# Kernel tuning notes

Hardware: AMD Instinct MI355X
Metric: run time of the kernel (lower is better)

Reference implementation:

```python
import jax, jax.numpy as jnp
import numpy as np
from jax.scipy.special import gammaln

D = 512       # feature_dim
C = 64        # n classes (n-way)
SHOTS = 5     # matches hardcoded self.fix_Nj = 5
Q = 2048      # query samples
FIX_NJ = 5.0


def setup_inputs() -> dict:
    key = jax.random.key(0)
    k1, k2 = jax.random.split(key, 2)
    X_support = jax.random.normal(k1, (C * SHOTS, D), dtype=jnp.float32)
    # labels 0..C-1, SHOTS contiguous samples per class (required: code indexes mu[j] by label)
    y = (jnp.arange(C * SHOTS, dtype=jnp.int32) // SHOTS)
    X_query = jax.random.normal(k2, (Q, D), dtype=jnp.float32)
    # learned parameters, initialized exactly as in the torch module
    m = jnp.zeros((1, D), dtype=jnp.float32)
    kappa = jnp.float32(0.1)
    nu = jnp.float32(D)
    triu_S_diag = jnp.ones((D,), dtype=jnp.float32)
    triu_S_lower = jnp.eye(D, dtype=jnp.float32)
    return {"X_support": X_support, "y": y, "X_query": X_query,
            "m": m, "kappa": kappa, "nu": nu,
            "triu_S_diag": triu_S_diag, "triu_S_lower": triu_S_lower}


def reference(X_support, y, X_query, m, kappa, nu, triu_S_diag, triu_S_lower):
    # ---- compute_shared_part ----
    # triu(ones,1).t() == strictly-lower-triangular mask
    mask = jnp.tril(jnp.ones((D, D), dtype=X_support.dtype), -1)
    L = jnp.diag(jnp.abs(triu_S_diag)) + triu_S_lower * mask
    kappa_n = jnp.abs(kappa) + 1e-6 + FIX_NJ
    m_with_weight = jnp.abs(kappa + 1e-6) / kappa_n * m          # [1,D]
    xmean_weight = FIX_NJ / kappa_n
    scatter = L @ L.T                                            # self_outer(L), square case
    sp = jnp.clip(nu, D - 1 + 1e-6) + FIX_NJ - D + 2             # sharedpart (scalar)
    bias_shared = gammaln(0.5 * (sp + D)) - gammaln(0.5 * sp) - 0.5 * D * jnp.log(sp)

    # ---- fit_image_label, batched over classes ----
    # y is arange//SHOTS so grouping X[y==j] == contiguous reshape
    Xc = X_support.reshape(C, SHOTS, D)                          # [C,S,D]
    x_mean = Xc.mean(axis=1)                                     # [C,D]
    mean_outer = jnp.einsum('csd,cse->cde', Xc, Xc) / SHOTS      # X_j^T X_j / N_j
    mu = m_with_weight + x_mean * xmean_weight                   # [C,D]
    dm = x_mean - m                                              # [C,D]; self_outer of [1,D] row -> outer product
    sigma = scatter[None] + mean_outer \
        + jnp.einsum('cd,ce->cde', dm, dm) * ((jnp.abs(kappa) + 1e-6) / kappa_n)
    sigma = sigma / ((kappa_n + 1) / (kappa_n * sp))             # [C,D,D]
    sigma_inv = jnp.linalg.inv(sigma)                            # batched inverse
    _, logdet = jnp.linalg.slogdet(sigma)                        # sigma is PD -> logdet
    biases = bias_shared - 0.5 * logdet                          # [C]

    # ---- predict, batched over queries and classes ----
    diff = X_query[:, None, :] - mu[None, :, :]                  # [Q,C,D]
    tmp = jnp.einsum('qcd,cde->qce', diff, sigma_inv)
    dist = jnp.sum(tmp * diff, axis=-1)                          # Mahalanobis [Q,C]
    return biases[None, :] - 0.5 * (sp + D) * jnp.log(1.0 + dist / sp)
```

## Files before the change

kernel.cpp:

```cpp
#include <hip/hip_runtime.h>
#include <math.h>

#define D 512
#define NC 64
#define NQ 2048

typedef unsigned short u16;
typedef __attribute__((ext_vector_type(8))) short bf8;
typedef __attribute__((ext_vector_type(4))) float f4;

#define OFF_S    0
#define OFF_ABH  32
#define OFF_ABL  (OFF_ABH + 655360)
#define OFF_LH   (OFF_ABL + 655360)
#define OFF_LL   (OFF_LH + 131072)
#define OFF_WH   (OFF_LL + 131072)
#define OFF_WL   (OFF_WH + 131072)
#define OFF_YYH  (OFF_WL + 131072)
#define OFF_YYL  (OFF_YYH + 655360)
#define OFF_AQ   (OFF_YYL + 655360)
#define OFF_GRAM (OFF_AQ + NQ)

#define GIX(i, j) ((i) * 7 - (i) * ((i) + 1) / 2 + (j))

__device__ inline float wred(float v) {
#pragma unroll
  for (int off = 32; off; off >>= 1) v += __shfl_down(v, off);
  return v;
}

__device__ inline void split2(float v, u16& h, u16& l) {
  unsigned u = __float_as_uint(v);
  h = (u16)(u >> 16);
  float hf = __uint_as_float(u & 0xFFFF0000u);
  float r = v - hf;
  unsigned ru = __float_as_uint(r);
  l = (u16)((ru + 0x7FFFu + ((ru >> 16) & 1u)) >> 16);
}

#define MPAD 68
template <int N>
__device__ inline void lds_mm(float (*M)[MPAD], int ar, int ac, int br, int bc,
                              int cr, int cc, bool neg) {
  const int T = N / 16;
  int tx = (threadIdx.x & 15) * T, ty = (threadIdx.x >> 4) * T;
  float acc[T][T];
#pragma unroll
  for (int i = 0; i < T; ++i)
#pragma unroll
    for (int j = 0; j < T; ++j) acc[i][j] = 0.f;
#pragma unroll 8
  for (int k = 0; k < N; ++k) {
    float a[T], b[T];
#pragma unroll
    for (int i = 0; i < T; ++i) a[i] = M[ar + ty + i][ac + k];
#pragma unroll
    for (int j = 0; j < T; ++j) b[j] = M[br + k][bc + tx + j];
#pragma unroll
    for (int i = 0; i < T; ++i)
#pragma unroll
      for (int j = 0; j < T; ++j) acc[i][j] += a[i] * b[j];
  }
#pragma unroll
  for (int i = 0; i < T; ++i)
#pragma unroll
    for (int j = 0; j < T; ++j)
      M[cr + ty + i][cc + tx + j] = neg ? -acc[i][j] : acc[i][j];
}

__global__ __launch_bounds__(256) void k_prep(const float* __restrict__ diag,
                                              const float* __restrict__ low,
                                              const float* __restrict__ Xs,
                                              const float* __restrict__ Xq,
                                              const float* __restrict__ m,
                                              const float* __restrict__ kp,
                                              const float* __restrict__ nup,
                                              u16* __restrict__ Lh, u16* __restrict__ Ll,
                                              u16* __restrict__ ABh, u16* __restrict__ ABl,
                                              u16* __restrict__ Wh, u16* __restrict__ Wl,
                                              float* __restrict__ S, float* __restrict__ aq,
                                              float* __restrict__ Gram) {
  __shared__ float M[64][MPAD];
  int bid = blockIdx.x, tid = threadIdx.x;
  if (bid < 1024) {
    int t = bid * 256 + tid;
    int i = t >> 9, j = t & 511;
    float v = (i == j) ? fabsf(diag[i]) : (i > j ? low[t] : 0.f);
    u16 hh, ll; split2(v, hh, ll);
    Lh[t] = hh; Ll[t] = ll;
    if (i < j) Wh[t] = 0;
  } else if (bid < 1088) {
    int c = bid - 1024;
    float kappa = kp[0];
    float kn = fabsf(kappa) + 1e-6f + 5.0f;
    float xw = 5.0f / kn;
    float mw = fabsf(kappa + 1e-6f) / kn;
    float sw = sqrtf((fabsf(kappa) + 1e-6f) / kn);
    const float is5 = 0.44721359549995793f;
    for (int d = tid; d < D; d += 256) {
      float x[5];
#pragma unroll
      for (int s = 0; s < 5; ++s) x[s] = Xs[(size_t)(c * 5 + s) * D + d];
      float xm = (x[0] + x[1] + x[2] + x[3] + x[4]) * 0.2f;
      float mv = m[d];
      float rowv[8];
#pragma unroll
      for (int s = 0; s < 5; ++s) rowv[s] = x[s] * is5;
      rowv[5] = sw * (xm - mv);
      rowv[6] = mw * mv + xw * xm;
      rowv[7] = 0.f;
#pragma unroll
      for (int s = 0; s < 8; ++s) {
        size_t gi = (size_t)(c * 8 + s) * D + d;
        u16 hh, ll; split2(rowv[s], hh, ll);
        ABh[gi] = hh; ABl[gi] = ll;
      }
    }
  } else if (bid == 1088) {
    for (int i = tid; i < NQ; i += 256) aq[i] = 0.f;
    for (int i = tid; i < NC * 28; i += 256) Gram[i] = 0.f;
    if (tid >= 64) return;
    float part = 0.f;
    for (int i = tid; i < D; i += 64) part += logf(fabsf(diag[i]));
    part = wred(part);
    if (tid != 0) return;
    float lda = 2.f * part;
    float kappa = kp[0], nu = nup[0];
    float kn = fabsf(kappa) + 1e-6f + 5.0f;
    float sp = fmaxf(nu, (float)(D - 1) + 1e-6f) + 5.0f - (float)D + 2.0f;
    float bias_shared = lgammaf(0.5f * (sp + (float)D)) - lgammaf(0.5f * sp)
                      - 0.5f * (float)D * logf(sp);
    float scale = kn * sp / (kn + 1.0f);
    S[3] = bias_shared;
    S[8] = 1.f / scale;
    S[9] = (float)D * logf(scale) + lda;
    S[10] = 0.5f * (sp + (float)D);
    S[11] = 1.f / sp;
  } else if (bid < 1601) {
    int idx = bid - 1089;
    size_t base = (size_t)512 * D + (size_t)idx * 2048;
    for (int i = tid; i < 2048; i += 256) {
      float v = Xq[(size_t)idx * 2048 + i];
      u16 hh, ll; split2(v, hh, ll);
      ABh[base + i] = hh; ABl[base + i] = ll;
    }
  } else {
    int p = (bid - 1601) * 64;
    for (int idx = tid; idx < 64 * 64; idx += 256) {
      int r = idx >> 6, c = idx & 63;
      float v;
      if (r == c)      v = fabsf(diag[p + r]);
      else if (r > c)  v = low[(size_t)(p + r) * D + p + c];
      else             v = 0.f;
      M[r][c] = v;
    }
    __syncthreads();
    {
      float x[16];
      int q = tid >> 4, col = tid & 15;
      if (tid < 64) {
        int b = q << 4;
#pragma unroll
        for (int i = 0; i < 16; ++i) {
          float acc = 0.f;
#pragma unroll
          for (int k = 0; k < i; ++k) acc += M[b + i][b + k] * x[k];
          x[i] = (((i == col) ? 1.f : 0.f) - acc) / M[b + i][b + i];
        }
      }
      __syncthreads();
      if (tid < 64) {
        int b = q << 4;
#pragma unroll
        for (int i = 0; i < 16; ++i) M[b + i][b + col] = x[i];
      }
      __syncthreads();
    }
    for (int pp = 0; pp < 2; ++pp) {
      int r0 = 32 * pp;
      lds_mm<16>(M, r0 + 16, r0, r0, r0, r0, r0 + 16, false);
    }
    __syncthreads();
    for (int pp = 0; pp < 2; ++pp) {
      int r0 = 32 * pp;
      lds_mm<16>(M, r0 + 16, r0 + 16, r0, r0 + 16, r0 + 16, r0, true);
    }
    __syncthreads();
    lds_mm<32>(M, 32, 0, 0, 0, 0, 32, false);
    __syncthreads();
    lds_mm<32>(M, 32, 32, 0, 32, 32, 0, true);
    __syncthreads();
    for (int idx = tid; idx < 64 * 64; idx += 256) {
      int r = idx >> 6, c = idx & 63;
      float v = (c > r) ? 0.f : M[r][c];
      u16 hh, ll; split2(v, hh, ll);
      size_t gi = (size_t)(p + r) * D + p + c;
      Wh[gi] = hh; Wl[gi] = ll;
    }
  }
}

__global__ __launch_bounds__(256) void k_solve(const u16* __restrict__ Lh,
                                               const u16* __restrict__ Ll,
                                               u16* __restrict__ Wh,
                                               u16* __restrict__ Wl) {
  __shared__ __align__(16) u16 XTh[32][520];
  __shared__ __align__(16) u16 XTl[32][520];
  __shared__ __align__(16) u16 STh[32][72];
  __shared__ __align__(16) u16 STl[32][72];
  int J = blockIdx.x;
  int i0 = J >> 1;
  int tid = threadIdx.x, w = tid >> 6, lane = tid & 63;
  int lr = lane & 15, kq = lane >> 4;
  for (int idx = tid; idx < 64 * 32; idx += 256) {
    int r = idx >> 5, c = idx & 31;
    size_t gi = (size_t)(64 * i0 + r) * D + 64 * i0 + (J & 1) * 32 + c;
    XTh[c][64 * i0 + r] = Wh[gi];
    XTl[c][64 * i0 + r] = Wl[gi];
  }
  __syncthreads();
  for (int i = i0 + 1; i < 8; ++i) {
    f4 acc[2];
    acc[0] = (f4){0.f, 0.f, 0.f, 0.f};
    acc[1] = (f4){0.f, 0.f, 0.f, 0.f};
    for (int k = i0; k < i; ++k) {
#pragma unroll
      for (int kk = 0; kk < 2; ++kk) {
        size_t ga = (size_t)(64 * i + w * 16 + lr) * D + 64 * k + kk * 32 + kq * 8;
        bf8 ah = *reinterpret_cast<const bf8*>(Lh + ga);
        bf8 al = *reinterpret_cast<const bf8*>(Ll + ga);
#pragma unroll
        for (int nf = 0; nf < 2; ++nf) {
          bf8 bh = *reinterpret_cast<const bf8*>(&XTh[nf * 16 + lr][64 * k + kk * 32 + kq * 8]);
          bf8 bl = *reinterpret_cast<const bf8*>(&XTl[nf * 16 + lr][64 * k + kk * 32 + kq * 8]);
          acc[nf] = __builtin_amdgcn_mfma_f32_16x16x32_bf16(ah, bh, acc[nf], 0, 0, 0);
          acc[nf] = __builtin_amdgcn_mfma_f32_16x16x32_bf16(ah, bl, acc[nf], 0, 0, 0);
          acc[nf] = __builtin_amdgcn_mfma_f32_16x16x32_bf16(al, bh, acc[nf], 0, 0, 0);
        }
      }
    }
#pragma unroll
    for (int nf = 0; nf < 2; ++nf)
#pragma unroll
      for (int reg = 0; reg < 4; ++reg) {
        float v = -acc[nf][reg];
        u16 hh, ll; split2(v, hh, ll);
        int c = nf * 16 + lr, r = w * 16 + kq * 4 + reg;
        STh[c][r] = hh; STl[c][r] = ll;
      }
    __syncthreads();
    f4 acc2[2];
    acc2[0] = (f4){0.f, 0.f, 0.f, 0.f};
    acc2[1] = (f4){0.f, 0.f, 0.f, 0.f};
#pragma unroll
    for (int kk = 0; kk < 2; ++kk) {
      size_t ga = (size_t)(64 * i + w * 16 + lr) * D + 64 * i + kk * 32 + kq * 8;
      bf8 ah = *reinterpret_cast<const bf8*>(Wh + ga);
      bf8 al = *reinterpret_cast<const bf8*>(Wl + ga);
#pragma unroll
      for (int nf = 0; nf < 2; ++nf) {
        bf8 bh = *reinterpret_cast<const bf8*>(&STh[nf * 16 + lr][kk * 32 + kq * 8]);
        bf8 bl = *reinterpret_cast<const bf8*>(&STl[nf * 16 + lr][kk * 32 + kq * 8]);
        acc2[nf] = __builtin_amdgcn_mfma_f32_16x16x32_bf16(ah, bh, acc2[nf], 0, 0, 0);
        acc2[nf] = __builtin_amdgcn_mfma_f32_16x16x32_bf16(ah, bl, acc2[nf], 0, 0, 0);
        acc2[nf] = __builtin_amdgcn_mfma_f32_16x16x32_bf16(al, bh, acc2[nf], 0, 0, 0);
      }
    }
#pragma unroll
    for (int nf = 0; nf < 2; ++nf)
#pragma unroll
      for (int reg = 0; reg < 4; ++reg) {
        float v = acc2[nf][reg];
        u16 hh, ll; split2(v, hh, ll);
        int r = w * 16 + kq * 4 + reg, c = nf * 16 + lr;
        size_t gi = (size_t)(64 * i + r) * D + 32 * J + c;
        Wh[gi] = hh;
        XTh[c][64 * i + r] = hh; XTl[c][64 * i + r] = ll;
      }
    __syncthreads();
  }
}

__global__ __launch_bounds__(256) void k_mf1(const u16* __restrict__ ABh, const u16* __restrict__ ABl,
                                             const u16* __restrict__ Wh,
                                             u16* __restrict__ YYh, u16* __restrict__ YYl,
                                             float* __restrict__ Gram, float* __restrict__ aq) {
  __shared__ float Csh[64][68];
  int tid = threadIdx.x, w = tid >> 6, lane = tid & 63;
  int m0 = blockIdx.x * 64 + w * 16;
  int bn = blockIdx.y * 64;
  int lr = lane & 15, kof = (lane >> 4) * 8;
  const u16* ah_p = ABh + (size_t)(m0 + lr) * D + kof;
  const u16* al_p = ABl + (size_t)(m0 + lr) * D + kof;
  const u16* bh_p = Wh + (size_t)(bn + lr) * D + kof;
  f4 acc[4];
#pragma unroll
  for (int nf = 0; nf < 4; ++nf) acc[nf] = (f4){0.f, 0.f, 0.f, 0.f};
  int Klim = bn + 64;
#pragma unroll 2
  for (int k0 = 0; k0 < Klim; k0 += 32) {
    bf8 ah = *reinterpret_cast<const bf8*>(ah_p + k0);
    bf8 al = *reinterpret_cast<const bf8*>(al_p + k0);
    bf8 bh[4];
#pragma unroll
    for (int nf = 0; nf < 4; ++nf)
      bh[nf] = *reinterpret_cast<const bf8*>(bh_p + (size_t)nf * 16 * D + k0);
#pragma unroll
    for (int nf = 0; nf < 4; ++nf)
      acc[nf] = __builtin_amdgcn_mfma_f32_16x16x32_bf16(ah, bh[nf], acc[nf], 0, 0, 0);
#pragma unroll
    for (int nf = 0; nf < 4; ++nf)
      acc[nf] = __builtin_amdgcn_mfma_f32_16x16x32_bf16(al, bh[nf], acc[nf], 0, 0, 0);
  }
  int rbase = m0 + ((lane >> 4) << 2);
#pragma unroll
  for (int reg = 0; reg < 4; ++reg) {
    int row = rbase + reg;
    float sq = 0.f;
#pragma unroll
    for (int nf = 0; nf < 4; ++nf) {
      float v = acc[nf][reg];
      size_t gi = (size_t)row * D + bn + nf * 16 + lr;
      u16 hh, ll; split2(v, hh, ll);
      YYh[gi] = hh;
      if (row >= 512) YYl[gi] = ll;
      sq += v * v;
    }
    if (row >= 512) {
#pragma unroll
      for (int mk = 1; mk < 16; mk <<= 1) sq += __shfl_xor(sq, mk);
      if (lr == 0) atomicAdd(&aq[row - 512], sq);
    }
  }
  if (blockIdx.x < 8) {
#pragma unroll
    for (int reg = 0; reg < 4; ++reg)
#pragma unroll
      for (int nf = 0; nf < 4; ++nf)
        Csh[w * 16 + ((lane >> 4) << 2) + reg][nf * 16 + lr] = acc[nf][reg];
    __syncthreads();
    if (tid < 224) {
      const int PI[28] = {0,0,0,0,0,0,0, 1,1,1,1,1,1, 2,2,2,2,2, 3,3,3,3, 4,4,4, 5,5, 6};
      const int PJ[28] = {0,1,2,3,4,5,6, 1,2,3,4,5,6, 2,3,4,5,6, 3,4,5,6, 4,5,6, 5,6, 6};
      int cl = tid / 28, p = tid % 28;
      const float* ri = Csh[cl * 8 + PI[p]];
      const float* rj = Csh[cl * 8 + PJ[p]];
      float s = 0.f;
#pragma unroll
      for (int c4 = 0; c4 < 64; c4 += 4) {
        float4 a = *reinterpret_cast<const float4*>(&ri[c4]);
        float4 b = *reinterpret_cast<const float4*>(&rj[c4]);
        s += a.x * b.x + a.y * b.y + a.z * b.z + a.w * b.w;
      }
      atomicAdd(&Gram[(blockIdx.x * 8 + cl) * 28 + p], s);
    }
  }
}

__global__ __launch_bounds__(256) void k_mf2(const u16* __restrict__ Yh, const u16* __restrict__ Yl,
                                             const u16* __restrict__ Bh,
                                             const float* __restrict__ aq,
                                             const float* __restrict__ Gram,
                                             const float* __restrict__ S,
                                             float* __restrict__ out) {
  __shared__ float Csh[4][16][68];
  __shared__ float PRo[8][15], PRd[8][6], Psv[8][6], Pb[8], Ph[8];
  int tid = threadIdx.x, w = tid >> 6, lane = tid & 63;
  int m0 = blockIdx.x * 64 + w * 16;
  int bn = blockIdx.y * 64;
  int lr = lane & 15, kof = (lane >> 4) * 8;
  const u16* ah_p = Yh + (size_t)(m0 + lr) * D + kof;
  const u16* al_p = Yl + (size_t)(m0 + lr) * D + kof;
  const u16* bh_p = Bh + (size_t)(bn + lr) * D + kof;
  f4 acc[4];
#pragma unroll
  for (int nf = 0; nf < 4; ++nf) acc[nf] = (f4){0.f, 0.f, 0.f, 0.f};
#pragma unroll 2
  for (int k0 = 0; k0 < D; k0 += 32) {
    bf8 ah = *reinterpret_cast<const bf8*>(ah_p + k0);
    bf8 al = *reinterpret_cast<const bf8*>(al_p + k0);
    bf8 bh[4];
#pragma unroll
    for (int nf = 0; nf < 4; ++nf)
      bh[nf] = *reinterpret_cast<const bf8*>(bh_p + (size_t)nf * 16 * D + k0);
#pragma unroll
    for (int nf = 0; nf < 4; ++nf)
      acc[nf] = __builtin_amdgcn_mfma_f32_16x16x32_bf16(ah, bh[nf], acc[nf], 0, 0, 0);
#pragma unroll
    for (int nf = 0; nf < 4; ++nf)
      acc[nf] = __builtin_amdgcn_mfma_f32_16x16x32_bf16(al, bh[nf], acc[nf], 0, 0, 0);
  }
#pragma unroll
  for (int reg = 0; reg < 4; ++reg)
#pragma unroll
    for (int nf = 0; nf < 4; ++nf)
      Csh[w][((lane >> 4) << 2) + reg][nf * 16 + lr] = acc[nf][reg];
  if (tid < 8) {
    int c = blockIdx.y * 8 + tid;
    float Gv[28];
#pragma unroll
    for (int p = 0; p < 28; ++p) Gv[p] = Gram[c * 28 + p];
    float R[6][6];
    float logdetM = 0.f;
#pragma unroll
    for (int i = 0; i < 6; ++i) {
      float s = Gv[GIX(i, i)] + 1.f;
#pragma unroll
      for (int k = 0; k < i; ++k) s -= R[i][k] * R[i][k];
      float rii = sqrtf(s);
      R[i][i] = rii;
      logdetM += logf(rii);
      float inv = 1.f / rii;
      PRd[tid][i] = inv;
#pragma unroll
      for (int r = i + 1; r < 6; ++r) {
        float s2 = Gv[GIX(i, r)];
#pragma unroll
        for (int k = 0; k < i; ++k) s2 -= R[r][k] * R[i][k];
        R[r][i] = s2 * inv;
      }
    }
#pragma unroll
    for (int i = 1; i < 6; ++i)
#pragma unroll
      for (int k = 0; k < i; ++k)
        PRo[tid][i * (i - 1) / 2 + k] = R[i][k];
#pragma unroll
    for (int j = 0; j < 6; ++j) Psv[tid][j] = Gv[GIX(j, 6)];
    Ph[tid] = Gv[27];
    Pb[tid] = S[3] - 0.5f * (S[9] + 2.f * logdetM);
  }
  __syncthreads();
  float s8 = S[8], s10 = S[10], s11 = S[11];
  int r = lr;
  int q = m0 + r;
  float aqv = aq[q];
#pragma unroll
  for (int cc = 0; cc < 2; ++cc) {
    int cl = ((lane >> 4) << 1) + cc;
    const float* t = &Csh[w][r][cl * 8];
    float e[6];
#pragma unroll
    for (int j = 0; j < 6; ++j) e[j] = t[j] - Psv[cl][j];
    const float* o = PRo[cl];
    const float* dg = PRd[cl];
    float z0 = e[0] * dg[0];
    float z1 = (e[1] - o[0] * z0) * dg[1];
    float z2 = (e[2] - o[1] * z0 - o[2] * z1) * dg[2];
    float z3 = (e[3] - o[3] * z0 - o[4] * z1 - o[5] * z2) * dg[3];
    float z4 = (e[4] - o[6] * z0 - o[7] * z1 - o[8] * z2 - o[9] * z3) * dg[4];
    float z5 = (e[5] - o[10] * z0 - o[11] * z1 - o[12] * z2 - o[13] * z3 - o[14] * z4) * dg[5];
    float quad = z0 * z0 + z1 * z1 + z2 * z2 + z3 * z3 + z4 * z4 + z5 * z5;
    float dist = (aqv - 2.f * t[6] + Ph[cl] - quad) * s8;
    out[(size_t)q * NC + blockIdx.y * 8 + cl] = Pb[cl] - s10 * log1pf(dist * s11);
  }
}

extern "C" void kernel_launch(void* const* d_in, const int* in_sizes, int n_in,
                              void* d_out, int out_size, void* d_ws, size_t ws_size,
                              hipStream_t stream) {
  const float* Xs   = (const float*)d_in[0];
  const float* Xq   = (const float*)d_in[2];
  const float* m    = (const float*)d_in[3];
  const float* kap  = (const float*)d_in[4];
  const float* nu   = (const float*)d_in[5];
  const float* diag = (const float*)d_in[6];
  const float* low  = (const float*)d_in[7];
  float* ws = (float*)d_ws;

  float* S    = ws + OFF_S;
  u16*   ABh  = (u16*)(ws + OFF_ABH);
  u16*   ABl  = (u16*)(ws + OFF_ABL);
  u16*   Lh   = (u16*)(ws + OFF_LH);
  u16*   Ll   = (u16*)(ws + OFF_LL);
  u16*   Wh   = (u16*)(ws + OFF_WH);
  u16*   Wl   = (u16*)(ws + OFF_WL);
  u16*   YYh  = (u16*)(ws + OFF_YYH);
  u16*   YYl  = (u16*)(ws + OFF_YYL);
  float* aq   = ws + OFF_AQ;
  float* Gram = ws + OFF_GRAM;

  hipLaunchKernelGGL(k_prep, dim3(1609), dim3(256), 0, stream,
                     diag, low, Xs, Xq, m, kap, nu, Lh, Ll, ABh, ABl, Wh, Wl, S, aq, Gram);
  hipLaunchKernelGGL(k_solve, dim3(16), dim3(256), 0, stream, Lh, Ll, Wh, Wl);
  hipLaunchKernelGGL(k_mf1, dim3(40, 8), dim3(256), 0, stream,
                     ABh, ABl, Wh, YYh, YYl, Gram, aq);
  hipLaunchKernelGGL(k_mf2, dim3(32, 8), dim3(256), 0, stream,
                     YYh + (size_t)512 * D, YYl + (size_t)512 * D, YYh,
                     aq, Gram, S, (float*)d_out);
}
```

Baseline: 80.00 us.

## Invert 128x128 diagonal blocks in prep and shorten blocked triangular solve chain

k_prep now inverts 128-wide diagonal blocks of L (two 64x64 inversions plus the off-diagonal coupling via LDS matmuls) instead of 64-wide blocks. k_solve then runs a 4-step block recurrence instead of an 8-step one, with each wave handling two 16-row MFMA tiles. This is meant to shorten the serial dependency chain in the 16-block solve kernel. In exchange, each prep block does more serial work and fewer blocks are launched. k_mf1's grid is also transposed and reversed so blocks sharing the same W column run together.

New measurement: 112.9 us. 41.1% more time.

```diff
diff --git a/kernel.cpp b/kernel.cpp
--- a/kernel.cpp
+++ b/kernel.cpp
@@ -66,6 +66,77 @@
 #pragma unroll
     for (int j = 0; j < T; ++j)
       M[cr + ty + i][cc + tx + j] = neg ? -acc[i][j] : acc[i][j];
+}
+
+__device__ inline void inv64(float (*M)[MPAD], int tid) {
+  {
+    float x[16];
+    int q = tid >> 4, col = tid & 15;
+    if (tid < 64) {
+      int b = q << 4;
+#pragma unroll
+      for (int i = 0; i < 16; ++i) {
+        float acc = 0.f;
+#pragma unroll
+        for (int k = 0; k < i; ++k) acc += M[b + i][b + k] * x[k];
+        x[i] = (((i == col) ? 1.f : 0.f) - acc) / M[b + i][b + i];
+      }
+    }
+    __syncthreads();
+    if (tid < 64) {
+      int b = q << 4;
+#pragma unroll
+      for (int i = 0; i < 16; ++i) M[b + i][b + col] = x[i];
+    }
+    __syncthreads();
+  }
+  for (int pp = 0; pp < 2; ++pp) {
+    int r0 = 32 * pp;
+    lds_mm<16>(M, r0 + 16, r0, r0, r0, r0, r0 + 16, false);
+  }
+  __syncthreads();
+  for (int pp = 0; pp < 2; ++pp) {
+    int r0 = 32 * pp;
+    lds_mm<16>(M, r0 + 16, r0 + 16, r0, r0 + 16, r0 + 16, r0, true);
+  }
+  __syncthreads();
+  for (int idx = tid; idx < 512; idx += 256) {
+    int t2 = idx >> 8, r = (idx >> 4) & 15, c = idx & 15;
+    M[32 * t2 + r][32 * t2 + 16 + c] = 0.f;
+  }
+  __syncthreads();
+  lds_mm<32>(M, 32, 0, 0, 0, 0, 32, false);
+  __syncthreads();
+  lds_mm<32>(M, 32, 32, 0, 32, 32, 0, true);
+  __syncthreads();
+  for (int idx = tid; idx < 1024; idx += 256) {
+    int r = idx >> 5, c = idx & 31;
+    M[r][32 + c] = 0.f;
+  }
+  __syncthreads();
+}
+
+__device__ inline void mm64(float (*Dst)[MPAD], const float (*A)[MPAD],
+                            const float (*B)[MPAD], bool neg, int tid) {
+  int tx = (tid & 15) * 4, ty = (tid >> 4) * 4;
+  float acc[4][4] = {};
+#pragma unroll 8
+  for (int k = 0; k < 64; ++k) {
+    float a[4], b[4];
+#pragma unroll
+    for (int i = 0; i < 4; ++i) a[i] = A[ty + i][k];
+#pragma unroll
+    for (int j = 0; j < 4; ++j) b[j] = B[k][tx + j];
+#pragma unroll
+    for (int i = 0; i < 4; ++i)
+#pragma unroll
+      for (int j = 0; j < 4; ++j) acc[i][j] += a[i] * b[j];
+  }
+#pragma unroll
+  for (int i = 0; i < 4; ++i)
+#pragma unroll
+    for (int j = 0; j < 4; ++j)
+      Dst[ty + i][tx + j] = neg ? -acc[i][j] : acc[i][j];
 }
 
 __global__ __launch_bounds__(256) void k_prep(const float* __restrict__ diag,
@@ -80,7 +151,7 @@
                                               u16* __restrict__ Wh, u16* __restrict__ Wl,
                                               float* __restrict__ S, float* __restrict__ aq,
                                               float* __restrict__ Gram) {
-  __shared__ float M[64][MPAD];
+  __shared__ float M3[3][64][MPAD];
   int bid = blockIdx.x, tid = threadIdx.x;
   if (bid < 1024) {
     int t = bid * 256 + tid;
@@ -88,7 +159,7 @@
     float v = (i == j) ? fabsf(diag[i]) : (i > j ? low[t] : 0.f);
     u16 hh, ll; split2(v, hh, ll);
     Lh[t] = hh; Ll[t] = ll;
-    if (i < j) Wh[t] = 0;
+    if (i < j) { Wh[t] = 0; Wl[t] = 0; }
   } else if (bid < 1088) {
     int c = bid - 1024;
     float kappa = kp[0];
@@ -145,57 +216,44 @@
       ABh[base + i] = hh; ABl[base + i] = ll;
     }
   } else {
-    int p = (bid - 1601) * 64;
-    for (int idx = tid; idx < 64 * 64; idx += 256) {
+    int p = (bid - 1601) * 128;
+    float (*b0)[MPAD] = M3[0];
+    float (*b1)[MPAD] = M3[1];
+    float (*b2)[MPAD] = M3[2];
+    for (int idx = tid; idx < 4096; idx += 256) {
       int r = idx >> 6, c = idx & 63;
-      float v;
-      if (r == c)      v = fabsf(diag[p + r]);
-      else if (r > c)  v = low[(size_t)(p + r) * D + p + c];
-      else             v = 0.f;
-      M[r][c] = v;
-    }
-    __syncthreads();
-    {
-      float x[16];
-      int q = tid >> 4, col = tid & 15;
-      if (tid < 64) {
-        int b = q << 4;
-#pragma unroll
-        for (int i = 0; i < 16; ++i) {
-          float acc = 0.f;
-#pragma unroll
-          for (int k = 0; k < i; ++k) acc += M[b + i][b + k] * x[k];
-          x[i] = (((i == col) ? 1.f : 0.f) - acc) / M[b + i][b + i];
-        }
-      }
-      __syncthreads();
-      if (tid < 64) {
-        int b = q << 4;
-#pragma unroll
-        for (int i = 0; i < 16; ++i) M[b + i][b + col] = x[i];
-      }
-      __syncthreads();
-    }
-    for (int pp = 0; pp < 2; ++pp) {
-      int r0 = 32 * pp;
-      lds_mm<16>(M, r0 + 16, r0, r0, r0, r0, r0 + 16, false);
-    }
-    __syncthreads();
-    for (int pp = 0; pp < 2; ++pp) {
-      int r0 = 32 * pp;
-      lds_mm<16>(M, r0 + 16, r0 + 16, r0, r0 + 16, r0 + 16, r0, true);
-    }
-    __syncthreads();
-    lds_mm<32>(M, 32, 0, 0, 0, 0, 32, false);
-    __syncthreads();
-    lds_mm<32>(M, 32, 32, 0, 32, 32, 0, true);
-    __syncthreads();
-    for (int idx = tid; idx < 64 * 64; idx += 256) {
+      b0[r][c] = (r == c) ? fabsf(diag[p + r])
+                          : (r > c ? low[(size_t)(p + r) * D + p + c] : 0.f);
+      b1[r][c] = low[(size_t)(p + 64 + r) * D + p + c];
+    }
+    __syncthreads();
+    inv64(b0, tid);
+    mm64(b2, b1, b0, false, tid);
+    __syncthreads();
+    for (int idx = tid; idx < 4096; idx += 256) {
       int r = idx >> 6, c = idx & 63;
-      float v = (c > r) ? 0.f : M[r][c];
-      u16 hh, ll; split2(v, hh, ll);
+      u16 hh, ll; split2(b0[r][c], hh, ll);
       size_t gi = (size_t)(p + r) * D + p + c;
       Wh[gi] = hh; Wl[gi] = ll;
+    }
+    for (int idx = tid; idx < 4096; idx += 256) {
+      int r = idx >> 6, c = idx & 63;
+      b1[r][c] = (r == c) ? fabsf(diag[p + 64 + r])
+                          : (r > c ? low[(size_t)(p + 64 + r) * D + p + 64 + c] : 0.f);
+    }
+    __syncthreads();
+    inv64(b1, tid);
+    mm64(b0, b1, b2, true, tid);
+    __syncthreads();
+    for (int idx = tid; idx < 4096; idx += 256) {
+      int r = idx >> 6, c = idx & 63;
+      u16 hh, ll;
+      split2(b1[r][c], hh, ll);
+      size_t gb = (size_t)(p + 64 + r) * D + p + 64 + c;
+      Wh[gb] = hh; Wl[gb] = ll;
+      split2(b0[r][c], hh, ll);
+      size_t gx = (size_t)(p + 64 + r) * D + p + c;
+      Wh[gx] = hh; Wl[gx] = ll;
     }
   }
 }
@@ -203,80 +261,93 @@
 __global__ __launch_bounds__(256) void k_solve(const u16* __restrict__ Lh,
                                                const u16* __restrict__ Ll,
                                                u16* __restrict__ Wh,
-                                               u16* __restrict__ Wl) {
+                                               const u16* __restrict__ Wl) {
   __shared__ __align__(16) u16 XTh[32][520];
   __shared__ __align__(16) u16 XTl[32][520];
-  __shared__ __align__(16) u16 STh[32][72];
-  __shared__ __align__(16) u16 STl[32][72];
+  __shared__ __align__(16) u16 STh[32][136];
+  __shared__ __align__(16) u16 STl[32][136];
   int J = blockIdx.x;
-  int i0 = J >> 1;
+  int i0 = J >> 2, cs = (J & 3) * 32;
   int tid = threadIdx.x, w = tid >> 6, lane = tid & 63;
   int lr = lane & 15, kq = lane >> 4;
-  for (int idx = tid; idx < 64 * 32; idx += 256) {
+  for (int idx = tid; idx < 128 * 32; idx += 256) {
     int r = idx >> 5, c = idx & 31;
-    size_t gi = (size_t)(64 * i0 + r) * D + 64 * i0 + (J & 1) * 32 + c;
-    XTh[c][64 * i0 + r] = Wh[gi];
-    XTl[c][64 * i0 + r] = Wl[gi];
-  }
-  __syncthreads();
-  for (int i = i0 + 1; i < 8; ++i) {
-    f4 acc[2];
-    acc[0] = (f4){0.f, 0.f, 0.f, 0.f};
-    acc[1] = (f4){0.f, 0.f, 0.f, 0.f};
+    size_t gi = (size_t)(128 * i0 + r) * D + 128 * i0 + cs + c;
+    XTh[c][128 * i0 + r] = Wh[gi];
+    XTl[c][128 * i0 + r] = Wl[gi];
+  }
+  __syncthreads();
+  for (int i = i0 + 1; i < 4; ++i) {
+    f4 acc[2][2];
+#pragma unroll
+    for (int mi = 0; mi < 2; ++mi)
+#pragma unroll
+      for (int nf = 0; nf < 2; ++nf) acc[mi][nf] = (f4){0.f, 0.f, 0.f, 0.f};
     for (int k = i0; k < i; ++k) {
 #pragma unroll
-      for (int kk = 0; kk < 2; ++kk) {
-        size_t ga = (size_t)(64 * i + w * 16 + lr) * D + 64 * k + kk * 32 + kq * 8;
-        bf8 ah = *reinterpret_cast<const bf8*>(Lh + ga);
-        bf8 al = *reinterpret_cast<const bf8*>(Ll + ga);
-#pragma unroll
-        for (int nf = 0; nf < 2; ++nf) {
-          bf8 bh = *reinterpret_cast<const bf8*>(&XTh[nf * 16 + lr][64 * k + kk * 32 + kq * 8]);
-          bf8 bl = *reinterpret_cast<const bf8*>(&XTl[nf * 16 + lr][64 * k + kk * 32 + kq * 8]);
-          acc[nf] = __builtin_amdgcn_mfma_f32_16x16x32_bf16(ah, bh, acc[nf], 0, 0, 0);
-          acc[nf] = __builtin_amdgcn_mfma_f32_16x16x32_bf16(ah, bl, acc[nf], 0, 0, 0);
-          acc[nf] = __builtin_amdgcn_mfma_f32_16x16x32_bf16(al, bh, acc[nf], 0, 0, 0);
+      for (int kf = 0; kf < 4; ++kf) {
+#pragma unroll
+        for (int mi = 0; mi < 2; ++mi) {
+          size_t ga = (size_t)(128 * i + (2 * w + mi) * 16 + lr) * D + 128 * k + kf * 32 + kq * 8;
+          bf8 ah = *reinterpret_cast<const bf8*>(Lh + ga);
+          bf8 al = *reinterpret_cast<const bf8*>(Ll + ga);
+#pragma unroll
+          for (int nf = 0; nf < 2; ++nf) {
+            bf8 bh = *reinterpret_cast<const bf8*>(&XTh[nf * 16 + lr][128 * k + kf * 32 + kq * 8]);
+            bf8 bl = *reinterpret_cast<const bf8*>(&XTl[nf * 16 + lr][128 * k + kf * 32 + kq * 8]);
+            acc[mi][nf] = __builtin_amdgcn_mfma_f32_16x16x32_bf16(ah, bh, acc[mi][nf], 0, 0, 0);
+            acc[mi][nf] = __builtin_amdgcn_mfma_f32_16x16x32_bf16(ah, bl, acc[mi][nf], 0, 0, 0);
+            acc[mi][nf] = __builtin_amdgcn_mfma_f32_16x16x32_bf16(al, bh, acc[mi][nf], 0, 0, 0);
+          }
         }
       }
     }
 #pragma unroll
-    for (int nf = 0; nf < 2; ++nf)
-#pragma unroll
-      for (int reg = 0; reg < 4; ++reg) {
-        float v = -acc[nf][reg];
-        u16 hh, ll; split2(v, hh, ll);
-        int c = nf * 16 + lr, r = w * 16 + kq * 4 + reg;
-        STh[c][r] = hh; STl[c][r] = ll;
+    for (int mi = 0; mi < 2; ++mi)
+#pragma unroll
+      for (int nf = 0; nf < 2; ++nf)
+#pragma unroll
+        for (int reg = 0; reg < 4; ++reg) {
+          float v = -acc[mi][nf][reg];
+          u16 hh, ll; split2(v, hh, ll);
+          int rl = (2 * w + mi) * 16 + kq * 4 + reg, cl = nf * 16 + lr;
+          STh[cl][rl] = hh; STl[cl][rl] = ll;
+        }
+    __syncthreads();
+    f4 acc2[2][2];
+#pragma unroll
+    for (int mi = 0; mi < 2; ++mi)
+#pragma unroll
+      for (int nf = 0; nf < 2; ++nf) acc2[mi][nf] = (f4){0.f, 0.f, 0.f, 0.f};
+#pragma unroll
+    for (int kf = 0; kf < 4; ++kf) {
+#pragma unroll
+      for (int mi = 0; mi < 2; ++mi) {
+        size_t ga = (size_t)(128 * i + (2 * w + mi) * 16 + lr) * D + 128 * i + kf * 32 + kq * 8;
+        bf8 ah = *reinterpret_cast<const bf8*>(Wh + ga);
+        bf8 al = *reinterpret_cast<const bf8*>(Wl + ga);
+#pragma unroll
+        for (int nf = 0; nf < 2; ++nf) {
+          bf8 bh = *reinterpret_cast<const bf8*>(&STh[nf * 16 + lr][kf * 32 + kq * 8]);
+          bf8 bl = *reinterpret_cast<const bf8*>(&STl[nf * 16 + lr][kf * 32 + kq * 8]);
+          acc2[mi][nf] = __builtin_amdgcn_mfma_f32_16x16x32_bf16(ah, bh, acc2[mi][nf], 0, 0, 0);
+          acc2[mi][nf] = __builtin_amdgcn_mfma_f32_16x16x32_bf16(ah, bl, acc2[mi][nf], 0, 0, 0);
+          acc2[mi][nf] = __builtin_amdgcn_mfma_f32_16x16x32_bf16(al, bh, acc2[mi][nf], 0, 0, 0);
+        }
       }
-    __syncthreads();
-    f4 acc2[2];
-    acc2[0] = (f4){0.f, 0.f, 0.f, 0.f};
-    acc2[1] = (f4){0.f, 0.f, 0.f, 0.f};
-#pragma unroll
-    for (int kk = 0; kk < 2; ++kk) {
-      size_t ga = (size_t)(64 * i + w * 16 + lr) * D + 64 * i + kk * 32 + kq * 8;
-      bf8 ah = *reinterpret_cast<const bf8*>(Wh + ga);
-      bf8 al = *reinterpret_cast<const bf8*>(Wl + ga);
-#pragma unroll
-      for (int nf = 0; nf < 2; ++nf) {
-        bf8 bh = *reinterpret_cast<const bf8*>(&STh[nf * 16 + lr][kk * 32 + kq * 8]);
-        bf8 bl = *reinterpret_cast<const bf8*>(&STl[nf * 16 + lr][kk * 32 + kq * 8]);
-        acc2[nf] = __builtin_amdgcn_mfma_f32_16x16x32_bf16(ah, bh, acc2[nf], 0, 0, 0);
-        acc2[nf] = __builtin_amdgcn_mfma_f32_16x16x32_bf16(ah, bl, acc2[nf], 0, 0, 0);
-        acc2[nf] = __builtin_amdgcn_mfma_f32_16x16x32_bf16(al, bh, acc2[nf], 0, 0, 0);
-      }
-    }
-#pragma unroll
-    for (int nf = 0; nf < 2; ++nf)
-#pragma unroll
-      for (int reg = 0; reg < 4; ++reg) {
-        float v = acc2[nf][reg];
-        u16 hh, ll; split2(v, hh, ll);
-        int r = w * 16 + kq * 4 + reg, c = nf * 16 + lr;
-        size_t gi = (size_t)(64 * i + r) * D + 32 * J + c;
-        Wh[gi] = hh;
-        XTh[c][64 * i + r] = hh; XTl[c][64 * i + r] = ll;
-      }
+    }
+#pragma unroll
+    for (int mi = 0; mi < 2; ++mi)
+#pragma unroll
+      for (int nf = 0; nf < 2; ++nf)
+#pragma unroll
+        for (int reg = 0; reg < 4; ++reg) {
+          float v = acc2[mi][nf][reg];
+          u16 hh, ll; split2(v, hh, ll);
+          int rl = (2 * w + mi) * 16 + kq * 4 + reg, cl = nf * 16 + lr;
+          Wh[(size_t)(128 * i + rl) * D + 32 * J + cl] = hh;
+          XTh[cl][128 * i + rl] = hh; XTl[cl][128 * i + rl] = ll;
+        }
     __syncthreads();
   }
 }
@@ -287,8 +358,8 @@
                                              float* __restrict__ Gram, float* __restrict__ aq) {
   __shared__ float Csh[64][68];
   int tid = threadIdx.x, w = tid >> 6, lane = tid & 63;
-  int m0 = blockIdx.x * 64 + w * 16;
-  int bn = blockIdx.y * 64;
+  int bn = (7 - (int)blockIdx.x) * 64;
+  int m0 = blockIdx.y * 64 + w * 16;
   int lr = lane & 15, kof = (lane >> 4) * 8;
   const u16* ah_p = ABh + (size_t)(m0 + lr) * D + kof;
   const u16* al_p = ABl + (size_t)(m0 + lr) * D + kof;
@@ -332,7 +403,7 @@
       if (lr == 0) atomicAdd(&aq[row - 512], sq);
     }
   }
-  if (blockIdx.x < 8) {
+  if (blockIdx.y < 8) {
 #pragma unroll
     for (int reg = 0; reg < 4; ++reg)
 #pragma unroll
@@ -352,7 +423,7 @@
         float4 b = *reinterpret_cast<const float4*>(&rj[c4]);
         s += a.x * b.x + a.y * b.y + a.z * b.z + a.w * b.w;
       }
-      atomicAdd(&Gram[(blockIdx.x * 8 + cl) * 28 + p], s);
+      atomicAdd(&Gram[(blockIdx.y * 8 + cl) * 28 + p], s);
     }
   }
 }
@@ -480,10 +551,10 @@
   float* aq   = ws + OFF_AQ;
   float* Gram = ws + OFF_GRAM;
 
-  hipLaunchKernelGGL(k_prep, dim3(1609), dim3(256), 0, stream,
+  hipLaunchKernelGGL(k_prep, dim3(1605), dim3(256), 0, stream,
                      diag, low, Xs, Xq, m, kap, nu, Lh, Ll, ABh, ABl, Wh, Wl, S, aq, Gram);
-  hipLaunchKernelGGL(k_solve, dim3(16), dim3(256), 0, stream, Lh, Ll, Wh, Wl);
-  hipLaunchKernelGGL(k_mf1, dim3(40, 8), dim3(256), 0, stream,
+  hipLaunchKernelGGL(k_solve, dim3(12), dim3(256), 0, stream, Lh, Ll, Wh, Wl);
+  hipLaunchKernelGGL(k_mf1, dim3(8, 40), dim3(256), 0, stream,
                      ABh, ABl, Wh, YYh, YYl, Gram, aq);
   hipLaunchKernelGGL(k_mf2, dim3(32, 8), dim3(256), 0, stream,
                      YYh + (size_t)512 * D, YYl + (size_t)512 * D, YYh,
```
